# Performance work log

Measured on AMD Instinct MI355X. Metric: run time of the kernel, lower is better.

The kernel has to match this reference:

```python
import jax, jax.numpy as jnp
import numpy as np

# Lorentz hyperboloid with curvature -1 (k = 1): <x,x>_L = -1/k, x0 = time coord.
K_CURV = 1.0
EPS = 1e-8
B, N, D, H = 4, 1024, 1024, 16
HD = D // H  # dim_per_head = 64 (space dims per head)


def _time(space):
    # time coord so the point lies on the hyperboloid
    return jnp.sqrt(jnp.sum(space * space, axis=-1, keepdims=True) + 1.0 / K_CURV)


def _lift(space):
    return jnp.concatenate([_time(space), space], axis=-1)


def _linner(u, v):
    # Minkowski inner product <u,v>_L = -u0 v0 + u_s . v_s
    return jnp.sum(u[..., 1:] * v[..., 1:], axis=-1) - u[..., 0] * v[..., 0]


def _lorentz_layernorm(x, gamma, beta):
    s = x[..., 1:]
    mu = jnp.mean(s, axis=-1, keepdims=True)
    var = jnp.mean((s - mu) ** 2, axis=-1, keepdims=True)
    s = (s - mu) / jnp.sqrt(var + 1e-5) * gamma + beta
    return _lift(s)


def _lorentz_linear(x, W, b):
    # linear on the full Lorentz point -> space part of output, time recomputed
    return _lift(x @ W + b)


def _lresnet(x, y, w):
    # Lorentzian residual: (x + w*y) renormalized back onto the hyperboloid
    z = x + w * y
    denom = jnp.sqrt(jnp.clip(-_linner(z, z), EPS))[..., None]
    return z / (jnp.sqrt(K_CURV) * denom)


def _attention(x, Wq, bq, Wk, bk, Wv, bv, Wo, bo):
    def heads(W, b):
        s = (x @ W + b).reshape(B, N, H, HD).transpose(0, 2, 1, 3)  # [B,H,N,HD]
        return _lift(s)  # per-head Lorentz points [B,H,N,HD+1]

    q, k, v = heads(Wq, bq), heads(Wk, bk), heads(Wv, bv)
    sgn = jnp.concatenate([-jnp.ones((1,), x.dtype), jnp.ones((HD,), x.dtype)])
    # pairwise Minkowski inner products; score = -d_L^2 = 2/k + 2<q,k>_L, scaled
    scores = jnp.einsum('bhqd,bhkd->bhqk', q * sgn, k)
    scores = (2.0 / K_CURV + 2.0 * scores) / np.sqrt(HD).astype(np.float32)
    attn = jax.nn.softmax(scores, axis=-1)
    # Lorentz midpoint aggregation of values
    mid = jnp.einsum('bhqk,bhkd->bhqd', attn, v)
    denom = jnp.sqrt(jnp.clip(-_linner(mid, mid), EPS))[..., None]
    mid = mid / (jnp.sqrt(K_CURV) * denom)  # [B,H,N,HD+1]
    cat = mid.transpose(0, 2, 1, 3).reshape(B, N, H * (HD + 1))  # trans_heads_concat
    return _lift(cat @ Wo + bo)


def reference(x, g1, b1, Wq, bq, Wk, bk, Wv, bv, Wo, bo, g2, b2, Wfc, bfc, Wpj, bpj, w1, w2):
    lx = _lorentz_layernorm(x, g1, b1)
    ax = _attention(lx, Wq, bq, Wk, bk, Wv, bv, Wo, bo)
    x = _lresnet(x, ax, w1)
    h = _lorentz_layernorm(x, g2, b2)
    h = _lorentz_linear(h, Wfc, bfc)                      # [B,N,4D]
    h = _lift(jax.nn.gelu(h[..., 1:], approximate=False))  # LorentzActivation(GELU)
    h = _lorentz_linear(h, Wpj, bpj)                      # [B,N,D]
    return _lresnet(x, h, w2)


def setup_inputs() -> dict:
    key = jax.random.key(0)
    ks = jax.random.split(key, 8)
    sc = 0.02
    f32 = jnp.float32
    xs = jax.random.normal(ks[0], (B, N, D - 1), f32)
    return dict(
        x=_lift(xs),
        g1=jnp.ones((D - 1,), f32), b1=jnp.zeros((D - 1,), f32),
        Wq=sc * jax.random.normal(ks[1], (D, H * HD), f32), bq=jnp.zeros((H * HD,), f32),
        Wk=sc * jax.random.normal(ks[2], (D, H * HD), f32), bk=jnp.zeros((H * HD,), f32),
        Wv=sc * jax.random.normal(ks[3], (D, H * HD), f32), bv=jnp.zeros((H * HD,), f32),
        Wo=sc * jax.random.normal(ks[4], (H * (HD + 1), D - 1), f32), bo=jnp.zeros((D - 1,), f32),
        g2=jnp.ones((D - 1,), f32), b2=jnp.zeros((D - 1,), f32),
        Wfc=sc * jax.random.normal(ks[5], (D, 4 * D - 1), f32), bfc=jnp.zeros((4 * D - 1,), f32),
        Wpj=sc * jax.random.normal(ks[6], (4 * D, D - 1), f32), bpj=jnp.zeros((D - 1,), f32),
        w1=jnp.ones((), f32), w2=jnp.ones((), f32),
    )
```

## Files before the change

### kernel.cpp

```cpp
#include <hip/hip_runtime.h>
#include <math.h>

#define BB 4
#define NN 1024
#define DD 1024
#define HH 16
#define ROWS (BB*NN)

typedef __attribute__((ext_vector_type(8))) short bf16x8;
typedef __attribute__((ext_vector_type(4))) float f32x4;
typedef unsigned short u16;

__device__ __forceinline__ u16 f2bf(float f) {
    union { float f; unsigned u; } v; v.f = f;
    unsigned r = v.u + 0x7fff + ((v.u >> 16) & 1);
    return (u16)(r >> 16);
}
__device__ __forceinline__ float bf2f(u16 u) {
    union { unsigned u; float f; } v; v.u = ((unsigned)u) << 16; return v.f;
}

__device__ __forceinline__ void async16(const void* g, void* l) {
    __builtin_amdgcn_global_load_lds(
        (__attribute__((address_space(1))) void*)(uintptr_t)g,
        (__attribute__((address_space(3))) void*)(uintptr_t)l,
        16, 0, 0);
}

__device__ __forceinline__ float block_reduce_sum(float v, float* sm) {
    #pragma unroll
    for (int o = 32; o > 0; o >>= 1) v += __shfl_down(v, o);
    int lane = threadIdx.x & 63, wid = threadIdx.x >> 6;
    if (lane == 0) sm[wid] = v;
    __syncthreads();
    if (wid == 0) {
        v = (lane < (int)(blockDim.x >> 6)) ? sm[lane] : 0.f;
        #pragma unroll
        for (int o = 2; o > 0; o >>= 1) v += __shfl_down(v, o);
        if (lane == 0) sm[0] = v;
    }
    __syncthreads();
    float r = sm[0];
    __syncthreads();
    return r;
}

__global__ __launch_bounds__(256) void k_pre(
        const float* __restrict__ Wq_, const float* __restrict__ Wk_,
        const float* __restrict__ Wv_, const float* __restrict__ Wo_,
        const float* __restrict__ Wfc_, const float* __restrict__ Wpj_,
        u16* __restrict__ WqkvT, u16* __restrict__ WoT,
        u16* __restrict__ WfcT, u16* __restrict__ WpjT,
        const float* __restrict__ x, const float* __restrict__ g1,
        const float* __restrict__ be1, u16* __restrict__ lnout) {
    __shared__ float t[32][33];
    int bid = blockIdx.x;
    if (bid < 12352) {
        const float* W; u16* out; int K, N, Kpad, Npad, gx;
        if (bid < 1024)      { W = Wq_;  out = WqkvT;            K = 1024; N = 1024; Kpad = 1024; Npad = 1024; gx = 32; }
        else if (bid < 2048) { W = Wk_;  out = WqkvT + 1048576;  K = 1024; N = 1024; Kpad = 1024; Npad = 1024; gx = 32; bid -= 1024; }
        else if (bid < 3072) { W = Wv_;  out = WqkvT + 2097152;  K = 1024; N = 1024; Kpad = 1024; Npad = 1024; gx = 32; bid -= 2048; }
        else if (bid < 4160) { W = Wo_;  out = WoT;              K = 1040; N = 1023; Kpad = 1088; Npad = 1024; gx = 34; bid -= 3072; }
        else if (bid < 8256) { W = Wfc_; out = WfcT;             K = 1024; N = 4095; Kpad = 1024; Npad = 4096; gx = 32; bid -= 4160; }
        else                 { W = Wpj_; out = WpjT;             K = 4096; N = 1023; Kpad = 4096; Npad = 1024; gx = 128; bid -= 8256; }
        int k0 = (bid % gx) * 32, n0 = (bid / gx) * 32;
        int tx = threadIdx.x & 31, ty = threadIdx.x >> 5;
        #pragma unroll
        for (int i = 0; i < 32; i += 8) {
            int k = k0 + ty + i, n = n0 + tx;
            t[ty + i][tx] = (k < K && n < N) ? W[(size_t)k * N + n] : 0.f;
        }
        __syncthreads();
        #pragma unroll
        for (int i = 0; i < 32; i += 8) {
            int n = n0 + ty + i, k = k0 + tx;
            if (n < Npad && k < Kpad) out[(size_t)n * Kpad + k] = f2bf(t[tx][ty + i]);
        }
    } else {
        float* sm = &t[0][0];
        int row = bid - 12352;
        const float* xr = x + (size_t)row * DD;
        u16* orow = lnout + (size_t)row * DD;
        float s = 0.f, ss = 0.f;
        for (int j = threadIdx.x; j < DD - 1; j += blockDim.x) {
            float v = xr[1 + j]; s += v; ss += v * v;
        }
        s = block_reduce_sum(s, sm);
        ss = block_reduce_sum(ss, sm);
        float mu = s / (float)(DD - 1);
        float var = ss / (float)(DD - 1) - mu * mu;
        float rstd = rsqrtf(var + 1e-5f);
        float s2 = 0.f;
        for (int j = threadIdx.x; j < DD - 1; j += blockDim.x) {
            float v = (xr[1 + j] - mu) * rstd * g1[j] + be1[j];
            orow[1 + j] = f2bf(v); s2 += v * v;
        }
        s2 = block_reduce_sum(s2, sm);
        if (threadIdx.x == 0) orow[0] = f2bf(sqrtf(s2 + 1.f));
    }
}

__device__ __forceinline__ void cstore(float* p, float v) { *p = v; }
__device__ __forceinline__ void cstore(u16* p, float v) { *p = f2bf(v); }

template <typename OT>
__global__ __launch_bounds__(256) void k_gemm_mfma(
        const u16* __restrict__ A, const u16* __restrict__ BT,
        const float* __restrict__ bias, int nbias,
        OT* __restrict__ C0, OT* __restrict__ C1,
        int ldc, int ldab, int ksplit, int K) {
    __shared__ __align__(16) u16 As[2][128 * 64];
    __shared__ __align__(16) u16 Bs[2][128 * 64];
    int z = blockIdx.z;
    int kbeg = z ? ksplit : 0;
    int kend = z ? K : ksplit;
    OT* C = z ? C1 : C0;
    const float* bs = z ? nullptr : bias;

    int tid = threadIdx.x;
    int wave = tid >> 6, lane = tid & 63;
    int quad = lane >> 4, m16 = lane & 15;
    int n0 = blockIdx.x * 128, m0 = blockIdx.y * 128;
    int wm = (wave & 1) * 64, wn = (wave >> 1) * 64;

    f32x4 acc[4][4];
    #pragma unroll
    for (int t = 0; t < 4; ++t)
        #pragma unroll
        for (int u = 0; u < 4; ++u) acc[t][u] = (f32x4){0.f, 0.f, 0.f, 0.f};

    int r8 = lane >> 3;
    int cc = (lane & 7) ^ r8;
    int srow = wave * 32 + r8;
    const u16* ag = A  + (size_t)(m0 + srow) * ldab + cc * 8;
    const u16* bg = BT + (size_t)(n0 + srow) * ldab + cc * 8;

    auto stage = [&](int k0, int s) {
        #pragma unroll
        for (int j = 0; j < 4; ++j) {
            async16(ag + (size_t)(j * 8) * ldab + k0, &As[s][(wave * 32 + j * 8) * 64]);
            async16(bg + (size_t)(j * 8) * ldab + k0, &Bs[s][(wave * 32 + j * 8) * 64]);
        }
    };

    int niter = (kend - kbeg) >> 6;
    stage(kbeg, 0);
    for (int it = 0; it < niter; ++it) {
        int cur = it & 1;
        __syncthreads();
        if (it + 1 < niter) stage(kbeg + (it + 1) * 64, cur ^ 1);
        #pragma unroll
        for (int kk = 0; kk < 2; ++kk) {
            bf16x8 af[4], bfr[4];
            #pragma unroll
            for (int t = 0; t < 4; ++t) {
                int slot = (kk * 4 + quad) ^ (m16 & 7);
                af[t] = *(const bf16x8*)&As[cur][(wm + t * 16 + m16) * 64 + slot * 8];
            }
            #pragma unroll
            for (int u = 0; u < 4; ++u) {
                int slot = (kk * 4 + quad) ^ (m16 & 7);
                bfr[u] = *(const bf16x8*)&Bs[cur][(wn + u * 16 + m16) * 64 + slot * 8];
            }
            #pragma unroll
            for (int t = 0; t < 4; ++t)
                #pragma unroll
                for (int u = 0; u < 4; ++u)
                    acc[t][u] = __builtin_amdgcn_mfma_f32_16x16x32_bf16(af[t], bfr[u], acc[t][u], 0, 0, 0);
        }
    }
    #pragma unroll
    for (int u = 0; u < 4; ++u) {
        int col = n0 + wn + u * 16 + m16;
        float bv = (bs != nullptr && col < nbias) ? bs[col] : 0.f;
        #pragma unroll
        for (int t = 0; t < 4; ++t) {
            #pragma unroll
            for (int r = 0; r < 4; ++r) {
                int row = m0 + wm + t * 16 + quad * 4 + r;
                cstore(C + (size_t)row * ldc + col, acc[t][u][r] + bv);
            }
        }
    }
}

__global__ __launch_bounds__(256) void k_build_heads(
        const u16* __restrict__ qkv,
        const float* __restrict__ bq, const float* __restrict__ bk,
        const float* __restrict__ bv,
        u16* __restrict__ Qp, u16* __restrict__ Kp, u16* __restrict__ V2) {
    int wid = threadIdx.x >> 6, lane = threadIdx.x & 63;
    int idx = blockIdx.x * 4 + wid;
    int h = idx & 15, bn = idx >> 4;
    int b = bn >> 10, n = bn & 1023;
    int sec = blockIdx.y;
    const float* bias = (sec == 0) ? bq : (sec == 1) ? bk : bv;
    float v = bf2f(qkv[(size_t)bn * 3072 + sec * 1024 + h * 64 + lane]) + bias[h * 64 + lane];
    float ss = v * v;
    #pragma unroll
    for (int o = 32; o > 0; o >>= 1) ss += __shfl_xor(ss, o);
    float tcomp = sqrtf(ss + 1.f);
    size_t bhn = (size_t)(b * 16 + h) * 1024 + n;
    if (sec == 0) {
        u16* drow = Qp + bhn * 96;
        drow[1 + lane] = f2bf(v);
        if (lane == 0) drow[0] = f2bf(-tcomp);
        if (lane < 31) drow[65 + lane] = 0;
    } else if (sec == 1) {
        u16* drow = Kp + bhn * 104;
        drow[1 + lane] = f2bf(v);
        if (lane == 0) drow[0] = f2bf(tcomp);
        if (lane < 39) drow[65 + lane] = 0;
    } else {
        u16* base = V2 + ((size_t)(b * 16 + h) * 16 + (n >> 6)) * 6144 + (n & 63);
        base[(1 + lane) * 72] = f2bf(v);
        if (lane == 0) base[0] = f2bf(tcomp);
        if (lane >= 49) base[(16 + lane) * 72] = 0;
    }
}

#define AKS 104
#define AVS 72
#define APS 88
#define KTILE_U16 (64 * AKS)
#define VTILE_U16 6144
#define EXPC 0.36067376f
__global__ __launch_bounds__(256) void k_attn_mfma(
        const u16* __restrict__ Qp, const u16* __restrict__ Kp,
        const u16* __restrict__ V2, u16* __restrict__ cat) {
    __shared__ __align__(16) u16 Klds[2][KTILE_U16];
    __shared__ __align__(16) u16 Vlds[2][VTILE_U16];
    __shared__ __align__(16) u16 Plds[4][16 * APS];
    int tid = threadIdx.x;
    int wave = tid >> 6, lane = tid & 63;
    int quad = lane >> 4, m = lane & 15;
    int bid = blockIdx.x;
    int bh = ((bid & 7) << 3) | (bid >> 6);
    int qt = (bid >> 3) & 7;

    const u16* kg = Kp + (size_t)bh * 16 * KTILE_U16;
    const u16* vg = V2 + (size_t)bh * 16 * VTILE_U16;

    bf16x8 aq[2][3];
    #pragma unroll
    for (int g = 0; g < 2; ++g) {
        const u16* qptr = Qp + ((size_t)bh * 1024 + qt * 128 + g * 64 + wave * 16 + m) * 96;
        aq[g][0] = *(const bf16x8*)(qptr + quad * 8);
        aq[g][1] = *(const bf16x8*)(qptr + 32 + quad * 8);
        aq[g][2] = *(const bf16x8*)(qptr + 64 + quad * 8);
    }

    f32x4 O[2][5];
    #pragma unroll
    for (int g = 0; g < 2; ++g)
        #pragma unroll
        for (int i = 0; i < 5; ++i) O[g][i] = (f32x4){0.f, 0.f, 0.f, 0.f};

    auto stage = [&](int kt, int s) {
        const u16* kt_p = kg + kt * KTILE_U16 + lane * 8;
        const u16* vt_p = vg + kt * VTILE_U16 + lane * 8;
        for (int i = wave; i < 25; i += 4) {
            if (i < 13) async16(kt_p + i * 512, &Klds[s][i * 512]);
            else        async16(vt_p + (i - 13) * 512, &Vlds[s][(i - 13) * 512]);
        }
    };

    stage(0, 0);
    for (int kt = 0; kt < 16; ++kt) {
        int cur = kt & 1;
        __syncthreads();
        if (kt < 15) stage(kt + 1, cur ^ 1);
        u16* pw = &Plds[wave][0];
        #pragma unroll
        for (int g = 0; g < 2; ++g) {
            #pragma unroll
            for (int nt = 0; nt < 4; ++nt) {
                f32x4 acc = (f32x4){0.f, 0.f, 0.f, 0.f};
                const u16* kr = &Klds[cur][(nt * 16 + m) * AKS + quad * 8];
                acc = __builtin_amdgcn_mfma_f32_16x16x32_bf16(*(const bf16x8*)(kr),      aq[g][0], acc, 0, 0, 0);
                acc = __builtin_amdgcn_mfma_f32_16x16x32_bf16(*(const bf16x8*)(kr + 32), aq[g][1], acc, 0, 0, 0);
                acc = __builtin_amdgcn_mfma_f32_16x16x32_bf16(*(const bf16x8*)(kr + 64), aq[g][2], acc, 0, 0, 0);
                unsigned pk0, pk1;
                {
                    union { float f; unsigned u; } a0, a1, a2, a3;
                    a0.f = __builtin_amdgcn_exp2f(fmaf(acc[0], EXPC, EXPC));
                    a1.f = __builtin_amdgcn_exp2f(fmaf(acc[1], EXPC, EXPC));
                    a2.f = __builtin_amdgcn_exp2f(fmaf(acc[2], EXPC, EXPC));
                    a3.f = __builtin_amdgcn_exp2f(fmaf(acc[3], EXPC, EXPC));
                    pk0 = ((a0.u + 0x8000u) >> 16) | (((a1.u + 0x8000u) >> 16) << 16);
                    pk1 = ((a2.u + 0x8000u) >> 16) | (((a3.u + 0x8000u) >> 16) << 16);
                }
                uint2 pk; pk.x = pk0; pk.y = pk1;
                *(uint2*)&pw[m * APS + nt * 16 + quad * 4] = pk;
            }
            #pragma unroll
            for (int kc = 0; kc < 2; ++kc) {
                bf16x8 ap = *(const bf16x8*)&Plds[wave][m * APS + kc * 32 + quad * 8];
                #pragma unroll
                for (int vt = 0; vt < 5; ++vt) {
                    bf16x8 bv = *(const bf16x8*)&Vlds[cur][(vt * 16 + m) * AVS + kc * 32 + quad * 8];
                    O[g][vt] = __builtin_amdgcn_mfma_f32_16x16x32_bf16(ap, bv, O[g][vt], 0, 0, 0);
                }
            }
        }
    }
    int b = bh >> 4, h = bh & 15;
    #pragma unroll
    for (int g = 0; g < 2; ++g) {
        #pragma unroll
        for (int r = 0; r < 4; ++r) {
            float part = 0.f;
            #pragma unroll
            for (int vt = 0; vt < 5; ++vt) {
                int c = vt * 16 + m;
                float o = O[g][vt][r];
                part += (c == 0) ? o * o : -o * o;
            }
            part += __shfl_xor(part, 1);
            part += __shfl_xor(part, 2);
            part += __shfl_xor(part, 4);
            part += __shfl_xor(part, 8);
            float rden = rsqrtf(fmaxf(part, 1e-8f));
            int n = qt * 128 + g * 64 + wave * 16 + quad * 4 + r;
            u16* crow = cat + (size_t)(b * 1024 + n) * 1088 + h * 65;
            #pragma unroll
            for (int vt = 0; vt < 5; ++vt) {
                int c = vt * 16 + m;
                if (c < 65) crow[c] = f2bf(O[g][vt][r] * rden);
            }
        }
    }
    if (h == 15) {
        for (int i = tid; i < 128 * 48; i += 256) {
            int rr = i / 48, c = i - rr * 48;
            int n = qt * 128 + rr;
            cat[(size_t)(b * 1024 + n) * 1088 + 1040 + c] = 0;
        }
    }
}

__global__ __launch_bounds__(256) void k_lresnet_ln(
        const float* __restrict__ x, const float* __restrict__ y0,
        const float* __restrict__ y1, const float* __restrict__ wscale,
        const float* __restrict__ g2, const float* __restrict__ be2,
        float* __restrict__ x1, u16* __restrict__ lnout) {
    __shared__ float sm[8];
    int row = blockIdx.x;
    const float* xr = x + (size_t)row * DD;
    const float* ya = y0 + (size_t)row * 1024;
    const float* yb = y1 + (size_t)row * 1024;
    float w = *wscale;
    float zreg[4];
    float sy = 0.f, sz = 0.f, szs = 0.f;
    int cnt = 0;
    for (int j = threadIdx.x; j < DD - 1; j += blockDim.x) {
        float yv = ya[j] + yb[j];
        float zv = xr[1 + j] + w * yv;
        sy += yv * yv; sz += zv * zv; szs += zv;
        zreg[cnt++] = zv;
    }
    sy = block_reduce_sum(sy, sm);
    sz = block_reduce_sum(sz, sm);
    szs = block_reduce_sum(szs, sm);
    float y0t = sqrtf(sy + 1.f);
    float z0 = xr[0] + w * y0t;
    float q = z0 * z0 - sz;
    float rden = rsqrtf(fmaxf(q, 1e-8f));
    float mu = rden * szs / (float)(DD - 1);
    float ex2 = rden * rden * sz / (float)(DD - 1);
    float var = ex2 - mu * mu;
    float rstd = rsqrtf(var + 1e-5f);
    float s2 = 0.f;
    cnt = 0;
    float* x1r = x1 + (size_t)row * DD;
    u16* lr = lnout + (size_t)row * DD;
    for (int j = threadIdx.x; j < DD - 1; j += blockDim.x) {
        float xv = zreg[cnt++] * rden;
        x1r[1 + j] = xv;
        float v = (xv - mu) * rstd * g2[j] + be2[j];
        lr[1 + j] = f2bf(v); s2 += v * v;
    }
    s2 = block_reduce_sum(s2, sm);
    if (threadIdx.x == 0) {
        x1r[0] = z0 * rden;
        lr[0] = f2bf(sqrtf(s2 + 1.f));
    }
}

__global__ __launch_bounds__(256) void k_lresnet(
        const float* __restrict__ x, const float* __restrict__ y0,
        const float* __restrict__ y1, const float* __restrict__ wscale,
        float* __restrict__ out) {
    __shared__ float sm[8];
    int row = blockIdx.x;
    const float* xr = x + (size_t)row * DD;
    const float* ya = y0 + (size_t)row * 1024;
    const float* yb = y1 + (size_t)row * 1024;
    float w = *wscale;
    float zreg[4];
    float sy = 0.f, sz = 0.f;
    int cnt = 0;
    for (int j = threadIdx.x; j < DD - 1; j += blockDim.x) {
        float yv = ya[j] + yb[j];
        float zv = xr[1 + j] + w * yv;
        sy += yv * yv; sz += zv * zv;
        zreg[cnt++] = zv;
    }
    sy = block_reduce_sum(sy, sm);
    sz = block_reduce_sum(sz, sm);
    float y0t = sqrtf(sy + 1.f);
    float z0 = xr[0] + w * y0t;
    float q = z0 * z0 - sz;
    float rden = rsqrtf(fmaxf(q, 1e-8f));
    cnt = 0;
    for (int j = threadIdx.x; j < DD - 1; j += blockDim.x)
        out[(size_t)row * DD + 1 + j] = zreg[cnt++] * rden;
    if (threadIdx.x == 0) out[(size_t)row * DD] = z0 * rden;
}

__global__ __launch_bounds__(256) void k_gelu_lift(
        const u16* __restrict__ hfc, u16* __restrict__ hg) {
    __shared__ float sm[8];
    int row = blockIdx.x;
    const u16* hr = hfc + (size_t)row * 4096;
    u16* gr = hg + (size_t)row * 4096;
    float s2 = 0.f;
    for (int j = threadIdx.x; j < 4095; j += blockDim.x) {
        float v = bf2f(hr[j]);
        float gl = 0.5f * v * (1.f + erff(v * 0.70710678f));
        gr[1 + j] = f2bf(gl); s2 += gl * gl;
    }
    s2 = block_reduce_sum(s2, sm);
    if (threadIdx.x == 0) gr[0] = f2bf(sqrtf(s2 + 1.f));
}

extern "C" void kernel_launch(void* const* d_in, const int* in_sizes, int n_in,
                              void* d_out, int out_size, void* d_ws, size_t ws_size,
                              hipStream_t stream) {
    const float* x   = (const float*)d_in[0];
    const float* g1  = (const float*)d_in[1];
    const float* b1  = (const float*)d_in[2];
    const float* Wq  = (const float*)d_in[3];
    const float* bq  = (const float*)d_in[4];
    const float* Wk  = (const float*)d_in[5];
    const float* bk  = (const float*)d_in[6];
    const float* Wv  = (const float*)d_in[7];
    const float* bv  = (const float*)d_in[8];
    const float* Wo  = (const float*)d_in[9];
    const float* bo  = (const float*)d_in[10];
    const float* g2  = (const float*)d_in[11];
    const float* b2  = (const float*)d_in[12];
    const float* Wfc = (const float*)d_in[13];
    const float* bfc = (const float*)d_in[14];
    const float* Wpj = (const float*)d_in[15];
    const float* bpj = (const float*)d_in[16];
    const float* w1  = (const float*)d_in[17];
    const float* w2  = (const float*)d_in[18];
    float* out = (float*)d_out;

    char* W = (char*)d_ws;
    u16* lx_bf  = (u16*)(W + 0);
    u16* WqkvT  = (u16*)(W + 8388608);
    u16* WoT    = (u16*)(W + 14680064);
    u16* WfcT   = (u16*)(W + 16908288);
    u16* WpjT   = (u16*)(W + 25296896);
    u16* qkv_bf = (u16*)(W + 33685504);
    u16* Qp     = (u16*)(W + 58851328);
    u16* Kp     = (u16*)(W + 71434240);
    u16* V2     = (u16*)(W + 85065728);
    u16* cat_bf = (u16*)(W + 97648640);
    float* ax0  = (float*)(W + 33685504);
    float* ax1  = (float*)(W + 50462720);
    float* x1   = (float*)(W + 67239936);
    u16* hfc_bf = (u16*)(W + 84017152);
    u16* hg_bf  = (u16*)(W + 33685504);
    float* h2a  = (float*)(W + 84017152);
    float* h2b  = (float*)(W + 100794368);

    dim3 blk(256);

    k_pre<<<16448, blk, 0, stream>>>(Wq, Wk, Wv, Wo, Wfc, Wpj,
                                     WqkvT, WoT, WfcT, WpjT,
                                     x, g1, b1, lx_bf);

    k_gemm_mfma<u16><<<dim3(24, 32, 1), blk, 0, stream>>>(
        lx_bf, WqkvT, nullptr, 0, qkv_bf, qkv_bf, 3072, 1024, 1024, 1024);
    k_build_heads<<<dim3(ROWS * HH / 4, 3), blk, 0, stream>>>(
        qkv_bf, bq, bk, bv, Qp, Kp, V2);

    k_attn_mfma<<<512, blk, 0, stream>>>(Qp, Kp, V2, cat_bf);

    k_gemm_mfma<float><<<dim3(8, 32, 2), blk, 0, stream>>>(
        cat_bf, WoT, bo, 1023, ax0, ax1, 1024, 1088, 576, 1088);

    k_lresnet_ln<<<ROWS, blk, 0, stream>>>(x, ax0, ax1, w1, g2, b2, x1, lx_bf);

    k_gemm_mfma<u16><<<dim3(32, 32, 1), blk, 0, stream>>>(
        lx_bf, WfcT, bfc, 4095, hfc_bf, hfc_bf, 4096, 1024, 1024, 1024);

    k_gelu_lift<<<ROWS, blk, 0, stream>>>(hfc_bf, hg_bf);

    k_gemm_mfma<float><<<dim3(8, 32, 2), blk, 0, stream>>>(
        hg_bf, WpjT, bpj, 1023, h2a, h2b, 1024, 4096, 2048, 4096);

    k_lresnet<<<ROWS, blk, 0, stream>>>(x1, h2a, h2b, w2, out);
}
```

Before: 434.1 us.

## Halve attention query tile per block and pass P via shuffles instead of LDS

The attention kernel now processes 64 queries per block instead of 128, doubling the grid to 1024 blocks for more parallelism across CUs. The probability tile is redistributed from the score accumulator layout to the MFMA A-operand layout using cross-lane shuffles rather than a round trip through a per-wave LDS buffer, which removes the P LDS allocation and its reads and writes. In exchange, each K/V tile staged into LDS is reused by half as many queries, doubling global K/V traffic, and each step adds shuffle instructions.

Measured after the change: 444.3 us. +2.4%, slower.

```diff
diff --git a/kernel.cpp b/kernel.cpp
--- a/kernel.cpp
+++ b/kernel.cpp
@@ -221,7 +221,6 @@
 
 #define AKS 104
 #define AVS 72
-#define APS 88
 #define KTILE_U16 (64 * AKS)
 #define VTILE_U16 6144
 #define EXPC 0.36067376f
@@ -230,31 +229,24 @@
         const u16* __restrict__ V2, u16* __restrict__ cat) {
     __shared__ __align__(16) u16 Klds[2][KTILE_U16];
     __shared__ __align__(16) u16 Vlds[2][VTILE_U16];
-    __shared__ __align__(16) u16 Plds[4][16 * APS];
     int tid = threadIdx.x;
     int wave = tid >> 6, lane = tid & 63;
     int quad = lane >> 4, m = lane & 15;
     int bid = blockIdx.x;
-    int bh = ((bid & 7) << 3) | (bid >> 6);
-    int qt = (bid >> 3) & 7;
+    int bh = ((bid & 7) << 3) | (bid >> 7);
+    int qt = (bid >> 3) & 15;
 
     const u16* kg = Kp + (size_t)bh * 16 * KTILE_U16;
     const u16* vg = V2 + (size_t)bh * 16 * VTILE_U16;
 
-    bf16x8 aq[2][3];
+    const u16* qptr = Qp + ((size_t)bh * 1024 + qt * 64 + wave * 16 + m) * 96;
+    bf16x8 aq0 = *(const bf16x8*)(qptr + quad * 8);
+    bf16x8 aq1 = *(const bf16x8*)(qptr + 32 + quad * 8);
+    bf16x8 aq2 = *(const bf16x8*)(qptr + 64 + quad * 8);
+
+    f32x4 O[5];
     #pragma unroll
-    for (int g = 0; g < 2; ++g) {
-        const u16* qptr = Qp + ((size_t)bh * 1024 + qt * 128 + g * 64 + wave * 16 + m) * 96;
-        aq[g][0] = *(const bf16x8*)(qptr + quad * 8);
-        aq[g][1] = *(const bf16x8*)(qptr + 32 + quad * 8);
-        aq[g][2] = *(const bf16x8*)(qptr + 64 + quad * 8);
-    }
-
-    f32x4 O[2][5];
-    #pragma unroll
-    for (int g = 0; g < 2; ++g)
-        #pragma unroll
-        for (int i = 0; i < 5; ++i) O[g][i] = (f32x4){0.f, 0.f, 0.f, 0.f};
+    for (int i = 0; i < 5; ++i) O[i] = (f32x4){0.f, 0.f, 0.f, 0.f};
 
     auto stage = [&](int kt, int s) {
         const u16* kt_p = kg + kt * KTILE_U16 + lane * 8;
@@ -265,75 +257,77 @@
         }
     };
 
+    int srcA = (quad & 1) * 32 + m;
+    int srcB = srcA + 16;
+    bool ntHi = (quad >> 1) != 0;
+
     stage(0, 0);
     for (int kt = 0; kt < 16; ++kt) {
         int cur = kt & 1;
         __syncthreads();
         if (kt < 15) stage(kt + 1, cur ^ 1);
-        u16* pw = &Plds[wave][0];
-        #pragma unroll
-        for (int g = 0; g < 2; ++g) {
+        uint2 pkk[4];
+        #pragma unroll
+        for (int nt = 0; nt < 4; ++nt) {
+            f32x4 acc = (f32x4){0.f, 0.f, 0.f, 0.f};
+            const u16* kr = &Klds[cur][(nt * 16 + m) * AKS + quad * 8];
+            acc = __builtin_amdgcn_mfma_f32_16x16x32_bf16(*(const bf16x8*)(kr),      aq0, acc, 0, 0, 0);
+            acc = __builtin_amdgcn_mfma_f32_16x16x32_bf16(*(const bf16x8*)(kr + 32), aq1, acc, 0, 0, 0);
+            acc = __builtin_amdgcn_mfma_f32_16x16x32_bf16(*(const bf16x8*)(kr + 64), aq2, acc, 0, 0, 0);
+            union { float f; unsigned u; } a0, a1, a2, a3;
+            a0.f = __builtin_amdgcn_exp2f(fmaf(acc[0], EXPC, EXPC));
+            a1.f = __builtin_amdgcn_exp2f(fmaf(acc[1], EXPC, EXPC));
+            a2.f = __builtin_amdgcn_exp2f(fmaf(acc[2], EXPC, EXPC));
+            a3.f = __builtin_amdgcn_exp2f(fmaf(acc[3], EXPC, EXPC));
+            pkk[nt].x = ((a0.u + 0x8000u) >> 16) | (((a1.u + 0x8000u) >> 16) << 16);
+            pkk[nt].y = ((a2.u + 0x8000u) >> 16) | (((a3.u + 0x8000u) >> 16) << 16);
+        }
+        #pragma unroll
+        for (int kc = 0; kc < 2; ++kc) {
+            uint2 lo = pkk[2 * kc], hi = pkk[2 * kc + 1];
+            unsigned d0a = __shfl((int)lo.x, srcA), d0b = __shfl((int)hi.x, srcA);
+            unsigned d1a = __shfl((int)lo.y, srcA), d1b = __shfl((int)hi.y, srcA);
+            unsigned d2a = __shfl((int)lo.x, srcB), d2b = __shfl((int)hi.x, srcB);
+            unsigned d3a = __shfl((int)lo.y, srcB), d3b = __shfl((int)hi.y, srcB);
+            union { uint4 u; bf16x8 v; } apu;
+            apu.u.x = ntHi ? d0b : d0a;
+            apu.u.y = ntHi ? d1b : d1a;
+            apu.u.z = ntHi ? d2b : d2a;
+            apu.u.w = ntHi ? d3b : d3a;
             #pragma unroll
-            for (int nt = 0; nt < 4; ++nt) {
-                f32x4 acc = (f32x4){0.f, 0.f, 0.f, 0.f};
-                const u16* kr = &Klds[cur][(nt * 16 + m) * AKS + quad * 8];
-                acc = __builtin_amdgcn_mfma_f32_16x16x32_bf16(*(const bf16x8*)(kr),      aq[g][0], acc, 0, 0, 0);
-                acc = __builtin_amdgcn_mfma_f32_16x16x32_bf16(*(const bf16x8*)(kr + 32), aq[g][1], acc, 0, 0, 0);
-                acc = __builtin_amdgcn_mfma_f32_16x16x32_bf16(*(const bf16x8*)(kr + 64), aq[g][2], acc, 0, 0, 0);
-                unsigned pk0, pk1;
-                {
-                    union { float f; unsigned u; } a0, a1, a2, a3;
-                    a0.f = __builtin_amdgcn_exp2f(fmaf(acc[0], EXPC, EXPC));
-                    a1.f = __builtin_amdgcn_exp2f(fmaf(acc[1], EXPC, EXPC));
-                    a2.f = __builtin_amdgcn_exp2f(fmaf(acc[2], EXPC, EXPC));
-                    a3.f = __builtin_amdgcn_exp2f(fmaf(acc[3], EXPC, EXPC));
-                    pk0 = ((a0.u + 0x8000u) >> 16) | (((a1.u + 0x8000u) >> 16) << 16);
-                    pk1 = ((a2.u + 0x8000u) >> 16) | (((a3.u + 0x8000u) >> 16) << 16);
-                }
-                uint2 pk; pk.x = pk0; pk.y = pk1;
-                *(uint2*)&pw[m * APS + nt * 16 + quad * 4] = pk;
-            }
-            #pragma unroll
-            for (int kc = 0; kc < 2; ++kc) {
-                bf16x8 ap = *(const bf16x8*)&Plds[wave][m * APS + kc * 32 + quad * 8];
-                #pragma unroll
-                for (int vt = 0; vt < 5; ++vt) {
-                    bf16x8 bv = *(const bf16x8*)&Vlds[cur][(vt * 16 + m) * AVS + kc * 32 + quad * 8];
-                    O[g][vt] = __builtin_amdgcn_mfma_f32_16x16x32_bf16(ap, bv, O[g][vt], 0, 0, 0);
-                }
+            for (int vt = 0; vt < 5; ++vt) {
+                bf16x8 bv = *(const bf16x8*)&Vlds[cur][(vt * 16 + m) * AVS + kc * 32 + quad * 8];
+                O[vt] = __builtin_amdgcn_mfma_f32_16x16x32_bf16(apu.v, bv, O[vt], 0, 0, 0);
             }
         }
     }
     int b = bh >> 4, h = bh & 15;
     #pragma unroll
-    for (int g = 0; g < 2; ++g) {
-        #pragma unroll
-        for (int r = 0; r < 4; ++r) {
-            float part = 0.f;
-            #pragma unroll
-            for (int vt = 0; vt < 5; ++vt) {
-                int c = vt * 16 + m;
-                float o = O[g][vt][r];
-                part += (c == 0) ? o * o : -o * o;
-            }
-            part += __shfl_xor(part, 1);
-            part += __shfl_xor(part, 2);
-            part += __shfl_xor(part, 4);
-            part += __shfl_xor(part, 8);
-            float rden = rsqrtf(fmaxf(part, 1e-8f));
-            int n = qt * 128 + g * 64 + wave * 16 + quad * 4 + r;
-            u16* crow = cat + (size_t)(b * 1024 + n) * 1088 + h * 65;
-            #pragma unroll
-            for (int vt = 0; vt < 5; ++vt) {
-                int c = vt * 16 + m;
-                if (c < 65) crow[c] = f2bf(O[g][vt][r] * rden);
-            }
+    for (int r = 0; r < 4; ++r) {
+        float part = 0.f;
+        #pragma unroll
+        for (int vt = 0; vt < 5; ++vt) {
+            int c = vt * 16 + m;
+            float o = O[vt][r];
+            part += (c == 0) ? o * o : -o * o;
+        }
+        part += __shfl_xor(part, 1);
+        part += __shfl_xor(part, 2);
+        part += __shfl_xor(part, 4);
+        part += __shfl_xor(part, 8);
+        float rden = rsqrtf(fmaxf(part, 1e-8f));
+        int n = qt * 64 + wave * 16 + quad * 4 + r;
+        u16* crow = cat + (size_t)(b * 1024 + n) * 1088 + h * 65;
+        #pragma unroll
+        for (int vt = 0; vt < 5; ++vt) {
+            int c = vt * 16 + m;
+            if (c < 65) crow[c] = f2bf(O[vt][r] * rden);
         }
     }
     if (h == 15) {
-        for (int i = tid; i < 128 * 48; i += 256) {
+        for (int i = tid; i < 64 * 48; i += 256) {
             int rr = i / 48, c = i - rr * 48;
-            int n = qt * 128 + rr;
+            int n = qt * 64 + rr;
             cat[(size_t)(b * 1024 + n) * 1088 + 1040 + c] = 0;
         }
     }
@@ -488,7 +482,7 @@
     k_build_heads<<<dim3(ROWS * HH / 4, 3), blk, 0, stream>>>(
         qkv_bf, bq, bk, bv, Qp, Kp, V2);
 
-    k_attn_mfma<<<512, blk, 0, stream>>>(Qp, Kp, V2, cat_bf);
+    k_attn_mfma<<<1024, blk, 0, stream>>>(Qp, Kp, V2, cat_bf);
 
     k_gemm_mfma<float><<<dim3(8, 32, 2), blk, 0, stream>>>(
         cat_bf, WoT, bo, 1023, ax0, ax1, 1024, 1088, 576, 1088);
```
